# Optimization experiments

Hardware: AMD Instinct MI355X
Metric: run time of the kernel (lower is better)

The kernel has to match this reference:

```python
import jax, jax.numpy as jnp
import numpy as np

DIM = 96; NH = 3; WS = 7; SHIFT = 3; P = 5; H = 56; W = 56
HEAD = DIM // NH; SCALE = HEAD ** -0.5
NWH = H // WS; NWW = W // WS; NW = NWH * NWW
TP = P * NW                 # total prompts = 320
N = P + WS * WS             # tokens per window incl. prompts = 54
HIDDEN = int(DIM * 4.0)


def _rel_pos_index():
    coords = np.stack(np.meshgrid(np.arange(WS), np.arange(WS), indexing='ij'))
    cf = coords.reshape(2, -1)
    rel = (cf[:, :, None] - cf[:, None, :]).transpose(1, 2, 0).astype(np.int64)
    rel[..., 0] += WS - 1
    rel[..., 1] += WS - 1
    rel[..., 0] *= 2 * WS - 1
    return rel.sum(-1)  # (49, 49)


def _attn_mask():
    img = np.zeros((H, W))
    cnt = 0
    sl = (slice(0, -WS), slice(-WS, -SHIFT), slice(-SHIFT, None))
    for hs in sl:
        for wsl in sl:
            img[hs, wsl] = cnt
            cnt += 1
    mw = img.reshape(NWH, WS, NWW, WS).transpose(0, 2, 1, 3).reshape(NW, WS * WS)
    am = mw[:, None, :] - mw[:, :, None]
    am = np.where(am != 0, -100.0, 0.0).astype(np.float32)
    # zero-pad for prompt rows/cols, matching the torch code's cat of zeros
    return np.pad(am, ((0, 0), (P, 0), (P, 0)))  # (NW, N, N)


RPI = _rel_pos_index()
MASK = jnp.asarray(_attn_mask())


def _ln(x, g, b):
    m = x.mean(-1, keepdims=True)
    v = ((x - m) ** 2).mean(-1, keepdims=True)
    return (x - m) / jnp.sqrt(v + 1e-5) * g + b


def setup_inputs() -> dict:
    key = jax.random.key(0)
    ks = jax.random.split(key, 10)
    B = 64
    s = DIM ** -0.5
    return {
        'x': jax.random.normal(ks[0], (B, H * W + TP, DIM), jnp.float32),
        'norm1_g': jnp.ones((DIM,), jnp.float32),
        'norm1_b': jnp.zeros((DIM,), jnp.float32),
        'qkv_w': jax.random.normal(ks[1], (DIM, 3 * DIM), jnp.float32) * s,
        'qkv_b': jnp.zeros((3 * DIM,), jnp.float32),
        'rpb_table': jax.random.normal(ks[2], ((2 * WS - 1) ** 2, NH), jnp.float32) * 0.02,
        'proj_w': jax.random.normal(ks[3], (DIM, DIM), jnp.float32) * s,
        'proj_b': jnp.zeros((DIM,), jnp.float32),
        'norm2_g': jnp.ones((DIM,), jnp.float32),
        'norm2_b': jnp.zeros((DIM,), jnp.float32),
        'fc1_w': jax.random.normal(ks[4], (DIM, HIDDEN), jnp.float32) * s,
        'fc1_b': jnp.zeros((HIDDEN,), jnp.float32),
        'fc2_w': jax.random.normal(ks[5], (HIDDEN, DIM), jnp.float32) * (HIDDEN ** -0.5),
        'fc2_b': jnp.zeros((DIM,), jnp.float32),
    }


def _block(x, norm1_g, norm1_b, qkv_w, qkv_b, rpb_table, proj_w, proj_b,
           norm2_g, norm2_b, fc1_w, fc1_b, fc2_w, fc2_b):
    B = x.shape[0]
    shortcut = x
    xn = _ln(x, norm1_g, norm1_b)

    prompt = xn[:, :TP, :]                       # (B, NW*P, C)
    feat = xn[:, TP:, :].reshape(B, H, W, DIM)
    feat = jnp.roll(feat, (-SHIFT, -SHIFT), (1, 2))

    # window partition -> (B*NW, WS*WS, C)
    xw = feat.reshape(B, NWH, WS, NWW, WS, DIM).transpose(0, 1, 3, 2, 4, 5)
    xw = xw.reshape(B * NW, WS * WS, DIM)
    # prepend per-window prompts
    xw = jnp.concatenate([prompt.reshape(B * NW, P, DIM), xw], axis=1)  # (B*NW, N, C)

    # attention
    qkv = (xw @ qkv_w + qkv_b).reshape(B * NW, N, 3, NH, HEAD).transpose(2, 0, 3, 1, 4)
    q, k, v = qkv[0] * SCALE, qkv[1], qkv[2]     # (B*NW, NH, N, HEAD)
    attn = jnp.einsum('bhnd,bhmd->bhnm', q, k)

    bias = rpb_table[RPI.reshape(-1)].reshape(WS * WS, WS * WS, NH).transpose(2, 0, 1)
    bias = jnp.pad(bias, ((0, 0), (P, 0), (P, 0)))  # (NH, N, N)
    attn = attn + bias[None]

    attn = attn.reshape(B, NW, NH, N, N) + MASK[None, :, None]
    attn = jax.nn.softmax(attn.reshape(B * NW, NH, N, N), axis=-1)

    out = jnp.einsum('bhnm,bhmd->bhnd', attn, v).transpose(0, 2, 1, 3).reshape(B * NW, N, DIM)
    out = out @ proj_w + proj_b

    prompt_out = out[:, :P, :].reshape(B, TP, DIM)
    fo = out[:, P:, :].reshape(B, NWH, NWW, WS, WS, DIM).transpose(0, 1, 3, 2, 4, 5)
    fo = fo.reshape(B, H, W, DIM)
    fo = jnp.roll(fo, (SHIFT, SHIFT), (1, 2))

    y = jnp.concatenate([prompt_out, fo.reshape(B, H * W, DIM)], axis=1)
    y = shortcut + y

    h = _ln(y, norm2_g, norm2_b)
    h = jax.nn.gelu(h @ fc1_w + fc1_b, approximate=False)
    y = y + (h @ fc2_w + fc2_b)
    return y


def reference(x, norm1_g, norm1_b, qkv_w, qkv_b, rpb_table, proj_w, proj_b,
              norm2_g, norm2_b, fc1_w, fc1_b, fc2_w, fc2_b):
    return _block(x, norm1_g, norm1_b, qkv_w, qkv_b, rpb_table, proj_w, proj_b,
                  norm2_g, norm2_b, fc1_w, fc1_b, fc2_w, fc2_b)
```

## Files before the change

### kernel.cpp

```cpp
#include <hip/hip_runtime.h>
#include <cmath>

typedef __bf16 bf16x8 __attribute__((ext_vector_type(8)));
typedef float  f32x4  __attribute__((ext_vector_type(4)));

#define MFMA16(a,b,c) __builtin_amdgcn_mfma_f32_16x16x32_bf16((a),(b),(c),0,0,0)

#define SCALE_Q 0.17677669529663687f

#define KST 104
#define VP  68


__global__ __launch_bounds__(256) void prep(const float* __restrict__ qkv_w,
                                            const float* __restrict__ proj_w,
                                            const float* __restrict__ fc1_w,
                                            const float* __restrict__ fc2_w,
                                            const float* __restrict__ rpb,
                                            __bf16* __restrict__ ws,
                                            float* __restrict__ tbl)
{
    int i = blockIdx.x * 256 + threadIdx.x;
    {
        int j = i;
        if (j < 27648) {
            int c = j / 96, k = j % 96;
            float v = qkv_w[k * 288 + c];
            if (c < 96) v *= SCALE_Q;
            ws[j] = (__bf16)v;
        } else if ((j -= 27648) < 9216) {
            int c = j / 96, k = j % 96;
            ws[27648 + j] = (__bf16)proj_w[k * 96 + c];
        } else if ((j -= 9216) < 36864) {
            int c = j / 96, k = j % 96;
            ws[36864 + j] = (__bf16)fc1_w[k * 384 + c];
        } else if ((j -= 36864) < 36864) {
            int c = j / 384, k = j % 384;
            ws[73728 + j] = (__bf16)fc2_w[k * 96 + c];
        }
    }
    if (i < 49152) {
        int n = i & 63, m = (i >> 6) & 63, h = (i >> 12) % 3, cls = i / 12288;
        float v;
        if (m >= 54) {
            v = -1e30f;
        } else {
            v = 0.f;
            if (n >= 5 && n < 54 && m >= 5) {
                int an = n - 5, am = m - 5;
                int iy = an / 7, ix = an % 7, jy = am / 7, jx = am % 7;
                v = rpb[((iy - jy + 6) * 13 + (ix - jx + 6)) * 3 + h];
                int whp = cls >> 1, wwp = cls & 1;
                int idn = (whp ? (iy < 4 ? 1 : 2) : 0) * 3 + (wwp ? (ix < 4 ? 1 : 2) : 0);
                int idm = (whp ? (jy < 4 ? 1 : 2) : 0) * 3 + (wwp ? (jx < 4 ? 1 : 2) : 0);
                if (idn != idm) v -= 100.f;
            }
        }
        tbl[i] = v;
    }
}

__device__ __forceinline__ int src_index(int b, int w, int wh, int ww, int t)
{
    if (t < 5) return b * 3456 + w * 5 + t;
    int a = t - 5;
    int hi = wh * 7 + a / 7 + 3; if (hi >= 56) hi -= 56;
    int wi = ww * 7 + a % 7 + 3; if (wi >= 56) wi -= 56;
    return b * 3456 + 320 + hi * 56 + wi;
}

__global__ __launch_bounds__(256, 2) void block_fused(const float* __restrict__ x,
                                                  const float* __restrict__ n1g, const float* __restrict__ n1b,
                                                  const float* __restrict__ qkvb, const float* __restrict__ tbl,
                                                  const float* __restrict__ projb,
                                                  const float* __restrict__ n2g, const float* __restrict__ n2b,
                                                  const float* __restrict__ fc1b, const float* __restrict__ fc2b,
                                                  const __bf16* __restrict__ wqkvT, const __bf16* __restrict__ wprojT,
                                                  const __bf16* __restrict__ w1T, const __bf16* __restrict__ w2T,
                                                  float* __restrict__ out)
{
    __shared__ __align__(16) char smem[79360];

    const int tid  = threadIdx.x;
    const int lane = tid & 63;
    const int wv   = tid >> 6;
    const int l15  = lane & 15;
    const int quad = lane >> 4;

    const int g  = blockIdx.x;
    const int b  = g >> 5;
    const int wp = g & 31;

    const int trow = wv * 16 + l15;

    __bf16* kt[2];  __bf16* vTp[2];  __bf16* sw[2];  float* obf[2];
    int wI[2], whI[2], wwI[2], clsI[2], tsrc[2];
    #pragma unroll
    for (int wx = 0; wx < 2; wx++) {
        kt[wx]  = (__bf16*)(smem + wx * 13312);
        vTp[wx] = (__bf16*)(smem + 26624 + wx * 13056);
        sw[wx]  = (__bf16*)(smem + 52736 + (wv * 2 + wx) * 3328);
        obf[wx] = (float*)(smem + wx * 25600);
        int w = wp * 2 + wx;
        wI[wx] = w;  whI[wx] = w >> 3;  wwI[wx] = w & 7;
        clsI[wx] = ((whI[wx] == 7) ? 2 : 0) + ((wwI[wx] == 7) ? 1 : 0);
        tsrc[wx] = src_index(b, w, whI[wx], wwI[wx], trow < 54 ? trow : 53);
    }

    bf16x8 xnfr[2][3];
    {
        float xv[2][24];
        #pragma unroll
        for (int wx = 0; wx < 2; wx++) {
            if (trow < 54) {
                const float* xr = x + (size_t)tsrc[wx] * 96 + quad * 8;
                #pragma unroll
                for (int ks = 0; ks < 3; ks++) {
                    float4 a0 = *(const float4*)(xr + ks * 32);
                    float4 a1 = *(const float4*)(xr + ks * 32 + 4);
                    float* p = xv[wx] + ks * 8;
                    p[0]=a0.x; p[1]=a0.y; p[2]=a0.z; p[3]=a0.w;
                    p[4]=a1.x; p[5]=a1.y; p[6]=a1.z; p[7]=a1.w;
                }
            } else {
                #pragma unroll
                for (int j = 0; j < 24; j++) xv[wx][j] = 0.f;
            }
        }
        float s[2] = {0.f, 0.f}, sq[2] = {0.f, 0.f};
        #pragma unroll
        for (int wx = 0; wx < 2; wx++)
            #pragma unroll
            for (int j = 0; j < 24; j++) { s[wx] += xv[wx][j]; sq[wx] += xv[wx][j] * xv[wx][j]; }
        #pragma unroll
        for (int wx = 0; wx < 2; wx++) { s[wx] += __shfl_xor(s[wx], 16, 64); sq[wx] += __shfl_xor(sq[wx], 16, 64); }
        #pragma unroll
        for (int wx = 0; wx < 2; wx++) { s[wx] += __shfl_xor(s[wx], 32, 64); sq[wx] += __shfl_xor(sq[wx], 32, 64); }
        float mean[2], rstd[2];
        #pragma unroll
        for (int wx = 0; wx < 2; wx++) {
            mean[wx] = s[wx] * (1.f / 96.f);
            rstd[wx] = rsqrtf(sq[wx] * (1.f / 96.f) - mean[wx] * mean[wx] + 1e-5f);
        }
        float keep = (trow < 54) ? 1.f : 0.f;
        #pragma unroll
        for (int ks = 0; ks < 3; ks++) {
            const float* gp = n1g + ks * 32 + quad * 8;
            const float* bp = n1b + ks * 32 + quad * 8;
            float4 g0 = *(const float4*)(gp), g1 = *(const float4*)(gp + 4);
            float4 b0 = *(const float4*)(bp), b1 = *(const float4*)(bp + 4);
            float gg[8] = {g0.x,g0.y,g0.z,g0.w,g1.x,g1.y,g1.z,g1.w};
            float bb[8] = {b0.x,b0.y,b0.z,b0.w,b1.x,b1.y,b1.z,b1.w};
            #pragma unroll
            for (int wx = 0; wx < 2; wx++)
                #pragma unroll
                for (int j = 0; j < 8; j++)
                    xnfr[wx][ks][j] = (__bf16)(((xv[wx][ks*8+j] - mean[wx]) * rstd[wx] * gg[j] + bb[j]) * keep);
        }
    }

    #pragma unroll
    for (int nt = 0; nt < 6; nt++) {
        const __bf16* br = wqkvT + (size_t)(nt * 16 + l15) * 96 + quad * 8;
        bf16x8 bf0 = *(const bf16x8*)(br);
        bf16x8 bf1 = *(const bf16x8*)(br + 32);
        bf16x8 bf2 = *(const bf16x8*)(br + 64);
        int col = nt * 16 + l15;
        float bias = qkvb[col] * SCALE_Q;
        #pragma unroll
        for (int wx = 0; wx < 2; wx++) {
            f32x4 acc = {0.f, 0.f, 0.f, 0.f};
            acc = MFMA16(xnfr[wx][0], bf0, acc);
            acc = MFMA16(xnfr[wx][1], bf1, acc);
            acc = MFMA16(xnfr[wx][2], bf2, acc);
            #pragma unroll
            for (int r = 0; r < 4; r++)
                sw[wx][(quad * 4 + r) * KST + col] = (__bf16)(acc[r] + bias);
        }
    }
    bf16x8 aq[2][3];
    #pragma unroll
    for (int wx = 0; wx < 2; wx++)
        #pragma unroll
        for (int h = 0; h < 3; h++)
            aq[wx][h] = *(const bf16x8*)(sw[wx] + l15 * KST + h * 32 + quad * 8);
    #pragma unroll
    for (int nt = 6; nt < 18; nt++) {
        const __bf16* br = wqkvT + (size_t)(nt * 16 + l15) * 96 + quad * 8;
        bf16x8 bf0 = *(const bf16x8*)(br);
        bf16x8 bf1 = *(const bf16x8*)(br + 32);
        bf16x8 bf2 = *(const bf16x8*)(br + 64);
        int col = nt * 16 + l15;
        float bias = qkvb[col];
        #pragma unroll
        for (int wx = 0; wx < 2; wx++) {
            f32x4 acc = {0.f, 0.f, 0.f, 0.f};
            acc = MFMA16(xnfr[wx][0], bf0, acc);
            acc = MFMA16(xnfr[wx][1], bf1, acc);
            acc = MFMA16(xnfr[wx][2], bf2, acc);
            if (nt < 12) {
                int kc = col - 96;
                #pragma unroll
                for (int r = 0; r < 4; r++)
                    kt[wx][(wv * 16 + quad * 4 + r) * KST + kc] = (__bf16)(acc[r] + bias);
            } else {
                int vc = col - 192;
                #pragma unroll
                for (int r = 0; r < 4; r++)
                    vTp[wx][vc * VP + (wv * 16 + quad * 4 + r)] = (__bf16)(acc[r] + bias);
            }
        }
    }
    __syncthreads();

    f32x4 oacc[2][6];
    #pragma unroll
    for (int wx = 0; wx < 2; wx++)
        #pragma unroll
        for (int i = 0; i < 6; i++) oacc[wx][i] = (f32x4){0.f, 0.f, 0.f, 0.f};

    #pragma unroll
    for (int h = 0; h < 3; h++) {
        float schv[2][4][4];
        #pragma unroll
        for (int wx = 0; wx < 2; wx++) {
            const float* tbT = tbl + (size_t)(clsI[wx] * 3 + h) * 4096;
            #pragma unroll
            for (int nt = 0; nt < 4; nt++) {
                bf16x8 bk = *(const bf16x8*)(kt[wx] + (nt * 16 + l15) * KST + h * 32 + quad * 8);
                f32x4 c = {0.f, 0.f, 0.f, 0.f};
                c = MFMA16(aq[wx][h], bk, c);
                float4 tv = *(const float4*)(tbT + (l15 + 16 * nt) * 64 + wv * 16 + quad * 4);
                schv[wx][nt][0] = c[0] + tv.x;
                schv[wx][nt][1] = c[1] + tv.y;
                schv[wx][nt][2] = c[2] + tv.z;
                schv[wx][nt][3] = c[3] + tv.w;
            }
        }
        #pragma unroll
        for (int r = 0; r < 4; r++) {
            float mx[2], e0[2], e1[2], e2[2], e3[2], sum[2];
            #pragma unroll
            for (int wx = 0; wx < 2; wx++)
                mx[wx] = fmaxf(fmaxf(schv[wx][0][r], schv[wx][1][r]), fmaxf(schv[wx][2][r], schv[wx][3][r]));
            #pragma unroll
            for (int d = 1; d < 16; d <<= 1)
                #pragma unroll
                for (int wx = 0; wx < 2; wx++) mx[wx] = fmaxf(mx[wx], __shfl_xor(mx[wx], d, 16));
            #pragma unroll
            for (int wx = 0; wx < 2; wx++) {
                e0[wx] = __expf(schv[wx][0][r] - mx[wx]);
                e1[wx] = __expf(schv[wx][1][r] - mx[wx]);
                e2[wx] = __expf(schv[wx][2][r] - mx[wx]);
                e3[wx] = __expf(schv[wx][3][r] - mx[wx]);
                sum[wx] = e0[wx] + e1[wx] + e2[wx] + e3[wx];
            }
            #pragma unroll
            for (int d = 1; d < 16; d <<= 1)
                #pragma unroll
                for (int wx = 0; wx < 2; wx++) sum[wx] += __shfl_xor(sum[wx], d, 16);
            #pragma unroll
            for (int wx = 0; wx < 2; wx++) {
                float inv = 1.f / sum[wx];
                __bf16* prw = sw[wx] + (quad * 4 + r) * VP + l15;
                prw[0]  = (__bf16)(e0[wx] * inv);
                prw[16] = (__bf16)(e1[wx] * inv);
                prw[32] = (__bf16)(e2[wx] * inv);
                prw[48] = (__bf16)(e3[wx] * inv);
            }
        }
        bf16x8 pa0[2], pa1[2];
        #pragma unroll
        for (int wx = 0; wx < 2; wx++) {
            pa0[wx] = *(const bf16x8*)(sw[wx] + l15 * VP + quad * 8);
            pa1[wx] = *(const bf16x8*)(sw[wx] + l15 * VP + 32 + quad * 8);
        }
        #pragma unroll
        for (int wx = 0; wx < 2; wx++)
            #pragma unroll
            for (int dt = 0; dt < 2; dt++) {
                const __bf16* vr = vTp[wx] + (h * 32 + dt * 16 + l15) * VP + quad * 8;
                f32x4 acc = oacc[wx][h * 2 + dt];
                acc = MFMA16(pa0[wx], *(const bf16x8*)(vr), acc);
                acc = MFMA16(pa1[wx], *(const bf16x8*)(vr + 32), acc);
                oacc[wx][h * 2 + dt] = acc;
            }
    }

    #pragma unroll
    for (int wx = 0; wx < 2; wx++)
        #pragma unroll
        for (int i = 0; i < 6; i++) {
            int colb = i * 16 + l15;
            #pragma unroll
            for (int r = 0; r < 4; r++)
                sw[wx][(quad * 4 + r) * KST + colb] = (__bf16)oacc[wx][i][r];
        }
    bf16x8 ofr[2][3];
    #pragma unroll
    for (int wx = 0; wx < 2; wx++)
        #pragma unroll
        for (int ks = 0; ks < 3; ks++)
            ofr[wx][ks] = *(const bf16x8*)(sw[wx] + l15 * KST + ks * 32 + quad * 8);

    __syncthreads();

    #pragma unroll
    for (int nt = 0; nt < 6; nt++) {
        const __bf16* br = wprojT + (size_t)(nt * 16 + l15) * 96 + quad * 8;
        bf16x8 bf0 = *(const bf16x8*)(br);
        bf16x8 bf1 = *(const bf16x8*)(br + 32);
        bf16x8 bf2 = *(const bf16x8*)(br + 64);
        int col = nt * 16 + l15;
        float pb = projb[col];
        #pragma unroll
        for (int wx = 0; wx < 2; wx++) {
            f32x4 acc = {0.f, 0.f, 0.f, 0.f};
            acc = MFMA16(ofr[wx][0], bf0, acc);
            acc = MFMA16(ofr[wx][1], bf1, acc);
            acc = MFMA16(ofr[wx][2], bf2, acc);
            #pragma unroll
            for (int r = 0; r < 4; r++)
                obf[wx][(wv * 16 + quad * 4 + r) * 100 + col] = acc[r] + pb;
        }
    }

    float yv[2][24];
    float s2[2] = {0.f, 0.f}, sq2[2] = {0.f, 0.f};
    #pragma unroll
    for (int wx = 0; wx < 2; wx++) {
        const float* xr = x + (size_t)tsrc[wx] * 96 + quad * 8;
        #pragma unroll
        for (int ks = 0; ks < 3; ks++) {
            float4 xa = *(const float4*)(xr + ks * 32);
            float4 xb = *(const float4*)(xr + ks * 32 + 4);
            float* ap = obf[wx] + trow * 100 + ks * 32 + quad * 8;
            float* yp = yv[wx] + ks * 8;
            yp[0] = xa.x + ap[0]; yp[1] = xa.y + ap[1]; yp[2] = xa.z + ap[2]; yp[3] = xa.w + ap[3];
            yp[4] = xb.x + ap[4]; yp[5] = xb.y + ap[5]; yp[6] = xb.z + ap[6]; yp[7] = xb.w + ap[7];
            #pragma unroll
            for (int j = 0; j < 8; j++) { s2[wx] += yp[j]; sq2[wx] += yp[j] * yp[j]; }
            ap[0] = yp[0]; ap[1] = yp[1]; ap[2] = yp[2]; ap[3] = yp[3];
            ap[4] = yp[4]; ap[5] = yp[5]; ap[6] = yp[6]; ap[7] = yp[7];
        }
    }
    #pragma unroll
    for (int wx = 0; wx < 2; wx++) { s2[wx] += __shfl_xor(s2[wx], 16, 64); sq2[wx] += __shfl_xor(sq2[wx], 16, 64); }
    #pragma unroll
    for (int wx = 0; wx < 2; wx++) { s2[wx] += __shfl_xor(s2[wx], 32, 64); sq2[wx] += __shfl_xor(sq2[wx], 32, 64); }
    float mean2[2], rstd2[2];
    #pragma unroll
    for (int wx = 0; wx < 2; wx++) {
        mean2[wx] = s2[wx] * (1.f / 96.f);
        rstd2[wx] = rsqrtf(sq2[wx] * (1.f / 96.f) - mean2[wx] * mean2[wx] + 1e-5f);
    }

    bf16x8 afr[2][3];
    #pragma unroll
    for (int ks = 0; ks < 3; ks++) {
        float4 g0 = *(const float4*)(n2g + ks * 32 + quad * 8);
        float4 g1 = *(const float4*)(n2g + ks * 32 + quad * 8 + 4);
        float4 b0 = *(const float4*)(n2b + ks * 32 + quad * 8);
        float4 b1 = *(const float4*)(n2b + ks * 32 + quad * 8 + 4);
        float gg[8] = {g0.x,g0.y,g0.z,g0.w,g1.x,g1.y,g1.z,g1.w};
        float bb[8] = {b0.x,b0.y,b0.z,b0.w,b1.x,b1.y,b1.z,b1.w};
        #pragma unroll
        for (int wx = 0; wx < 2; wx++)
            #pragma unroll
            for (int j = 0; j < 8; j++)
                afr[wx][ks][j] = (__bf16)((yv[wx][ks*8+j] - mean2[wx]) * rstd2[wx] * gg[j] + bb[j]);
    }

    bf16x8 hfr[2][12];
    #pragma unroll
    for (int np = 0; np < 12; np++) {
        #pragma unroll
        for (int u = 0; u < 2; u++) {
            int ntx = np * 2 + u;
            const __bf16* br = w1T + (size_t)(ntx * 16 + l15) * 96 + quad * 8;
            bf16x8 bf0 = *(const bf16x8*)(br);
            bf16x8 bf1 = *(const bf16x8*)(br + 32);
            bf16x8 bf2 = *(const bf16x8*)(br + 64);
            float fb = fc1b[ntx * 16 + l15];
            #pragma unroll
            for (int wx = 0; wx < 2; wx++) {
                f32x4 acc = {0.f, 0.f, 0.f, 0.f};
                acc = MFMA16(afr[wx][0], bf0, acc);
                acc = MFMA16(afr[wx][1], bf1, acc);
                acc = MFMA16(afr[wx][2], bf2, acc);
                #pragma unroll
                for (int r = 0; r < 4; r++) {
                    float v  = acc[r] + fb;
                    float u2 = -1.5957691216057308f * v * (1.f + 0.044715f * v * v);
                    float t  = __expf(u2);
                    float ge = v * __builtin_amdgcn_rcpf(1.f + t);
                    sw[wx][(quad * 4 + r) * 40 + u * 16 + l15] = (__bf16)ge;
                }
            }
        }
        #pragma unroll
        for (int wx = 0; wx < 2; wx++)
            hfr[wx][np] = *(const bf16x8*)(sw[wx] + l15 * 40 + quad * 8);
    }

    #pragma unroll
    for (int nt = 0; nt < 6; nt++) {
        int col = nt * 16 + l15;
        const __bf16* br = w2T + (size_t)col * 384 + quad * 8;
        float fb = fc2b[col];
        f32x4 acc0 = {0.f, 0.f, 0.f, 0.f};
        f32x4 acc1 = {0.f, 0.f, 0.f, 0.f};
        #pragma unroll
        for (int ks = 0; ks < 12; ks++) {
            bf16x8 bb = *(const bf16x8*)(br + ks * 32);
            acc0 = MFMA16(hfr[0][ks], bb, acc0);
            acc1 = MFMA16(hfr[1][ks], bb, acc1);
        }
        #pragma unroll
        for (int r = 0; r < 4; r++) {
            obf[0][(wv * 16 + quad * 4 + r) * 100 + col] += acc0[r] + fb;
            obf[1][(wv * 16 + quad * 4 + r) * 100 + col] += acc1[r] + fb;
        }
    }

    #pragma unroll
    for (int wx = 0; wx < 2; wx++)
        #pragma unroll
        for (int it = 0; it < 6; it++) {
            int i = it * 64 + lane;
            int rr = i / 24, seg = i - rr * 24;
            int row = wv * 16 + rr;
            if (row < 54) {
                int src = src_index(b, wI[wx], whI[wx], wwI[wx], row);
                const float* sp = obf[wx] + row * 100 + seg * 4;
                float4 v = make_float4(sp[0], sp[1], sp[2], sp[3]);
                *(float4*)(out + (size_t)src * 96 + seg * 4) = v;
            }
        }
}

extern "C" void kernel_launch(void* const* d_in, const int* in_sizes, int n_in,
                              void* d_out, int out_size, void* d_ws, size_t ws_size,
                              hipStream_t stream)
{
    const float* x      = (const float*)d_in[0];
    const float* n1g    = (const float*)d_in[1];
    const float* n1b    = (const float*)d_in[2];
    const float* qkv_w  = (const float*)d_in[3];
    const float* qkv_b  = (const float*)d_in[4];
    const float* rpb    = (const float*)d_in[5];
    const float* proj_w = (const float*)d_in[6];
    const float* proj_b = (const float*)d_in[7];
    const float* n2g    = (const float*)d_in[8];
    const float* n2b    = (const float*)d_in[9];
    const float* fc1_w  = (const float*)d_in[10];
    const float* fc1_b  = (const float*)d_in[11];
    const float* fc2_w  = (const float*)d_in[12];
    const float* fc2_b  = (const float*)d_in[13];

    __bf16* ws     = (__bf16*)d_ws;
    __bf16* wqkvT  = ws;
    __bf16* wprojT = ws + 27648;
    __bf16* w1T    = ws + 36864;
    __bf16* w2T    = ws + 73728;
    float*  tbl    = (float*)((char*)d_ws + 221184);

    float* out = (float*)d_out;

    hipLaunchKernelGGL(prep, dim3(432), dim3(256), 0, stream,
                       qkv_w, proj_w, fc1_w, fc2_w, rpb, ws, tbl);
    hipLaunchKernelGGL(block_fused, dim3(2048), dim3(256), 0, stream,
                       x, n1g, n1b, qkv_b, tbl, proj_b, n2g, n2b, fc1_b, fc2_b,
                       wqkvT, wprojT, w1T, w2T, out);
}
```

Baseline: 357.4 us.

## Swap MFMA operand order to keep row-major token outputs in registers

Swaps the A/B operands of most MFMAs so each lane holds four consecutive output columns of one token row. This allows packed bf16x4 LDS stores, keeps the projection and residual outputs in registers instead of an fp32 LDS staging buffer, and writes the final output straight from registers. The softmax now reduces across lanes with two cross-quad shuffles instead of four 16-lane ones. fc1 and fc2 are interleaved so fc2 accumulates chunk by chunk without holding all hidden fragments, and one __syncthreads is dropped. The cost is higher register pressure from the acc2 and yv arrays, and the bias table is re-indexed to match the transposed score layout.

```diff
diff --git a/kernel.cpp b/kernel.cpp
--- a/kernel.cpp
+++ b/kernel.cpp
@@ -2,11 +2,13 @@
 #include <cmath>
 
 typedef __bf16 bf16x8 __attribute__((ext_vector_type(8)));
+typedef __bf16 bf16x4 __attribute__((ext_vector_type(4)));
 typedef float  f32x4  __attribute__((ext_vector_type(4)));
 
 #define MFMA16(a,b,c) __builtin_amdgcn_mfma_f32_16x16x32_bf16((a),(b),(c),0,0,0)
 
 #define SCALE_Q 0.17677669529663687f
+
 
 #define KST 104
 #define VP  68
@@ -40,14 +42,14 @@
         }
     }
     if (i < 49152) {
-        int n = i & 63, m = (i >> 6) & 63, h = (i >> 12) % 3, cls = i / 12288;
+        int k_ = i & 63, q_ = (i >> 6) & 63, h = (i >> 12) % 3, cls = i / 12288;
         float v;
-        if (m >= 54) {
+        if (k_ >= 54) {
             v = -1e30f;
         } else {
             v = 0.f;
-            if (n >= 5 && n < 54 && m >= 5) {
-                int an = n - 5, am = m - 5;
+            if (q_ >= 5 && q_ < 54 && k_ >= 5) {
+                int an = q_ - 5, am = k_ - 5;
                 int iy = an / 7, ix = an % 7, jy = am / 7, jx = am % 7;
                 v = rpb[((iy - jy + 6) * 13 + (ix - jx + 6)) * 3 + h];
                 int whp = cls >> 1, wwp = cls & 1;
@@ -93,14 +95,13 @@
 
     const int trow = wv * 16 + l15;
 
-    __bf16* kt[2];  __bf16* vTp[2];  __bf16* sw[2];  float* obf[2];
+    __bf16* kt[2];  __bf16* vTp[2];  __bf16* sw[2];
     int wI[2], whI[2], wwI[2], clsI[2], tsrc[2];
     #pragma unroll
     for (int wx = 0; wx < 2; wx++) {
         kt[wx]  = (__bf16*)(smem + wx * 13312);
         vTp[wx] = (__bf16*)(smem + 26624 + wx * 13056);
         sw[wx]  = (__bf16*)(smem + 52736 + (wv * 2 + wx) * 3328);
-        obf[wx] = (float*)(smem + wx * 25600);
         int w = wp * 2 + wx;
         wI[wx] = w;  whI[wx] = w >> 3;  wwI[wx] = w & 7;
         clsI[wx] = ((whI[wx] == 7) ? 2 : 0) + ((wwI[wx] == 7) ? 1 : 0);
@@ -136,46 +137,47 @@
         for (int wx = 0; wx < 2; wx++) { s[wx] += __shfl_xor(s[wx], 16, 64); sq[wx] += __shfl_xor(sq[wx], 16, 64); }
         #pragma unroll
         for (int wx = 0; wx < 2; wx++) { s[wx] += __shfl_xor(s[wx], 32, 64); sq[wx] += __shfl_xor(sq[wx], 32, 64); }
-        float mean[2], rstd[2];
-        #pragma unroll
-        for (int wx = 0; wx < 2; wx++) {
-            mean[wx] = s[wx] * (1.f / 96.f);
-            rstd[wx] = rsqrtf(sq[wx] * (1.f / 96.f) - mean[wx] * mean[wx] + 1e-5f);
-        }
         float keep = (trow < 54) ? 1.f : 0.f;
         #pragma unroll
-        for (int ks = 0; ks < 3; ks++) {
-            const float* gp = n1g + ks * 32 + quad * 8;
-            const float* bp = n1b + ks * 32 + quad * 8;
-            float4 g0 = *(const float4*)(gp), g1 = *(const float4*)(gp + 4);
-            float4 b0 = *(const float4*)(bp), b1 = *(const float4*)(bp + 4);
-            float gg[8] = {g0.x,g0.y,g0.z,g0.w,g1.x,g1.y,g1.z,g1.w};
-            float bb[8] = {b0.x,b0.y,b0.z,b0.w,b1.x,b1.y,b1.z,b1.w};
-            #pragma unroll
-            for (int wx = 0; wx < 2; wx++)
+        for (int wx = 0; wx < 2; wx++) {
+            float mean = s[wx] * (1.f / 96.f);
+            float rstd = rsqrtf(sq[wx] * (1.f / 96.f) - mean * mean + 1e-5f);
+            #pragma unroll
+            for (int ks = 0; ks < 3; ks++) {
+                const float* gp = n1g + ks * 32 + quad * 8;
+                const float* bp = n1b + ks * 32 + quad * 8;
+                float4 g0 = *(const float4*)(gp), g1 = *(const float4*)(gp + 4);
+                float4 b0 = *(const float4*)(bp), b1 = *(const float4*)(bp + 4);
+                float gg[8] = {g0.x,g0.y,g0.z,g0.w,g1.x,g1.y,g1.z,g1.w};
+                float bb[8] = {b0.x,b0.y,b0.z,b0.w,b1.x,b1.y,b1.z,b1.w};
                 #pragma unroll
                 for (int j = 0; j < 8; j++)
-                    xnfr[wx][ks][j] = (__bf16)(((xv[wx][ks*8+j] - mean[wx]) * rstd[wx] * gg[j] + bb[j]) * keep);
-        }
-    }
-
-    #pragma unroll
-    for (int nt = 0; nt < 6; nt++) {
+                    xnfr[wx][ks][j] = (__bf16)(((xv[wx][ks*8+j] - mean) * rstd * gg[j] + bb[j]) * keep);
+            }
+        }
+    }
+
+    #pragma unroll
+    for (int nt = 0; nt < 12; nt++) {
         const __bf16* br = wqkvT + (size_t)(nt * 16 + l15) * 96 + quad * 8;
-        bf16x8 bf0 = *(const bf16x8*)(br);
-        bf16x8 bf1 = *(const bf16x8*)(br + 32);
-        bf16x8 bf2 = *(const bf16x8*)(br + 64);
-        int col = nt * 16 + l15;
-        float bias = qkvb[col] * SCALE_Q;
+        bf16x8 b0 = *(const bf16x8*)(br);
+        bf16x8 b1 = *(const bf16x8*)(br + 32);
+        bf16x8 b2 = *(const bf16x8*)(br + 64);
+        float4 bias4 = *(const float4*)(qkvb + nt * 16 + quad * 4);
+        if (nt < 6) { bias4.x *= SCALE_Q; bias4.y *= SCALE_Q; bias4.z *= SCALE_Q; bias4.w *= SCALE_Q; }
         #pragma unroll
         for (int wx = 0; wx < 2; wx++) {
             f32x4 acc = {0.f, 0.f, 0.f, 0.f};
-            acc = MFMA16(xnfr[wx][0], bf0, acc);
-            acc = MFMA16(xnfr[wx][1], bf1, acc);
-            acc = MFMA16(xnfr[wx][2], bf2, acc);
-            #pragma unroll
-            for (int r = 0; r < 4; r++)
-                sw[wx][(quad * 4 + r) * KST + col] = (__bf16)(acc[r] + bias);
+            acc = MFMA16(b0, xnfr[wx][0], acc);
+            acc = MFMA16(b1, xnfr[wx][1], acc);
+            acc = MFMA16(b2, xnfr[wx][2], acc);
+            bf16x4 pk;
+            pk[0] = (__bf16)(acc[0] + bias4.x);
+            pk[1] = (__bf16)(acc[1] + bias4.y);
+            pk[2] = (__bf16)(acc[2] + bias4.z);
+            pk[3] = (__bf16)(acc[3] + bias4.w);
+            if (nt < 6) *(bf16x4*)(sw[wx] + l15 * KST + nt * 16 + quad * 4) = pk;
+            else        *(bf16x4*)(kt[wx] + (size_t)trow * KST + (nt - 6) * 16 + quad * 4) = pk;
         }
     }
     bf16x8 aq[2][3];
@@ -184,31 +186,27 @@
         #pragma unroll
         for (int h = 0; h < 3; h++)
             aq[wx][h] = *(const bf16x8*)(sw[wx] + l15 * KST + h * 32 + quad * 8);
-    #pragma unroll
-    for (int nt = 6; nt < 18; nt++) {
+
+    #pragma unroll
+    for (int nt = 12; nt < 18; nt++) {
         const __bf16* br = wqkvT + (size_t)(nt * 16 + l15) * 96 + quad * 8;
-        bf16x8 bf0 = *(const bf16x8*)(br);
-        bf16x8 bf1 = *(const bf16x8*)(br + 32);
-        bf16x8 bf2 = *(const bf16x8*)(br + 64);
-        int col = nt * 16 + l15;
-        float bias = qkvb[col];
+        bf16x8 b0 = *(const bf16x8*)(br);
+        bf16x8 b1 = *(const bf16x8*)(br + 32);
+        bf16x8 b2 = *(const bf16x8*)(br + 64);
+        float bias = qkvb[nt * 16 + l15];
+        int vc = nt * 16 + l15 - 192;
         #pragma unroll
         for (int wx = 0; wx < 2; wx++) {
             f32x4 acc = {0.f, 0.f, 0.f, 0.f};
-            acc = MFMA16(xnfr[wx][0], bf0, acc);
-            acc = MFMA16(xnfr[wx][1], bf1, acc);
-            acc = MFMA16(xnfr[wx][2], bf2, acc);
-            if (nt < 12) {
-                int kc = col - 96;
-                #pragma unroll
-                for (int r = 0; r < 4; r++)
-                    kt[wx][(wv * 16 + quad * 4 + r) * KST + kc] = (__bf16)(acc[r] + bias);
-            } else {
-                int vc = col - 192;
-                #pragma unroll
-                for (int r = 0; r < 4; r++)
-                    vTp[wx][vc * VP + (wv * 16 + quad * 4 + r)] = (__bf16)(acc[r] + bias);
-            }
+            acc = MFMA16(xnfr[wx][0], b0, acc);
+            acc = MFMA16(xnfr[wx][1], b1, acc);
+            acc = MFMA16(xnfr[wx][2], b2, acc);
+            bf16x4 pk;
+            pk[0] = (__bf16)(acc[0] + bias);
+            pk[1] = (__bf16)(acc[1] + bias);
+            pk[2] = (__bf16)(acc[2] + bias);
+            pk[3] = (__bf16)(acc[3] + bias);
+            *(bf16x4*)(vTp[wx] + (size_t)vc * VP + wv * 16 + quad * 4) = pk;
         }
     }
     __syncthreads();
@@ -221,107 +219,99 @@
 
     #pragma unroll
     for (int h = 0; h < 3; h++) {
-        float schv[2][4][4];
-        #pragma unroll
-        for (int wx = 0; wx < 2; wx++) {
-            const float* tbT = tbl + (size_t)(clsI[wx] * 3 + h) * 4096;
+        float sv[2][4][4];
+        #pragma unroll
+        for (int wx = 0; wx < 2; wx++) {
+            const float* tbh = tbl + (size_t)(clsI[wx] * 3 + h) * 4096 + trow * 64 + quad * 4;
             #pragma unroll
             for (int nt = 0; nt < 4; nt++) {
-                bf16x8 bk = *(const bf16x8*)(kt[wx] + (nt * 16 + l15) * KST + h * 32 + quad * 8);
+                bf16x8 ak = *(const bf16x8*)(kt[wx] + (nt * 16 + l15) * KST + h * 32 + quad * 8);
                 f32x4 c = {0.f, 0.f, 0.f, 0.f};
-                c = MFMA16(aq[wx][h], bk, c);
-                float4 tv = *(const float4*)(tbT + (l15 + 16 * nt) * 64 + wv * 16 + quad * 4);
-                schv[wx][nt][0] = c[0] + tv.x;
-                schv[wx][nt][1] = c[1] + tv.y;
-                schv[wx][nt][2] = c[2] + tv.z;
-                schv[wx][nt][3] = c[3] + tv.w;
-            }
-        }
-        #pragma unroll
-        for (int r = 0; r < 4; r++) {
-            float mx[2], e0[2], e1[2], e2[2], e3[2], sum[2];
-            #pragma unroll
-            for (int wx = 0; wx < 2; wx++)
-                mx[wx] = fmaxf(fmaxf(schv[wx][0][r], schv[wx][1][r]), fmaxf(schv[wx][2][r], schv[wx][3][r]));
-            #pragma unroll
-            for (int d = 1; d < 16; d <<= 1)
-                #pragma unroll
-                for (int wx = 0; wx < 2; wx++) mx[wx] = fmaxf(mx[wx], __shfl_xor(mx[wx], d, 16));
-            #pragma unroll
-            for (int wx = 0; wx < 2; wx++) {
-                e0[wx] = __expf(schv[wx][0][r] - mx[wx]);
-                e1[wx] = __expf(schv[wx][1][r] - mx[wx]);
-                e2[wx] = __expf(schv[wx][2][r] - mx[wx]);
-                e3[wx] = __expf(schv[wx][3][r] - mx[wx]);
-                sum[wx] = e0[wx] + e1[wx] + e2[wx] + e3[wx];
-            }
-            #pragma unroll
-            for (int d = 1; d < 16; d <<= 1)
-                #pragma unroll
-                for (int wx = 0; wx < 2; wx++) sum[wx] += __shfl_xor(sum[wx], d, 16);
-            #pragma unroll
-            for (int wx = 0; wx < 2; wx++) {
-                float inv = 1.f / sum[wx];
-                __bf16* prw = sw[wx] + (quad * 4 + r) * VP + l15;
-                prw[0]  = (__bf16)(e0[wx] * inv);
-                prw[16] = (__bf16)(e1[wx] * inv);
-                prw[32] = (__bf16)(e2[wx] * inv);
-                prw[48] = (__bf16)(e3[wx] * inv);
-            }
-        }
-        bf16x8 pa0[2], pa1[2];
-        #pragma unroll
-        for (int wx = 0; wx < 2; wx++) {
-            pa0[wx] = *(const bf16x8*)(sw[wx] + l15 * VP + quad * 8);
-            pa1[wx] = *(const bf16x8*)(sw[wx] + l15 * VP + 32 + quad * 8);
-        }
-        #pragma unroll
-        for (int wx = 0; wx < 2; wx++)
+                c = MFMA16(ak, aq[wx][h], c);
+                float4 tv = *(const float4*)(tbh + nt * 16);
+                sv[wx][nt][0] = c[0] + tv.x;
+                sv[wx][nt][1] = c[1] + tv.y;
+                sv[wx][nt][2] = c[2] + tv.z;
+                sv[wx][nt][3] = c[3] + tv.w;
+            }
+        }
+        #pragma unroll
+        for (int wx = 0; wx < 2; wx++) {
+            float mx = sv[wx][0][0];
+            #pragma unroll
+            for (int nt = 0; nt < 4; nt++)
+                #pragma unroll
+                for (int r = 0; r < 4; r++) mx = fmaxf(mx, sv[wx][nt][r]);
+            mx = fmaxf(mx, __shfl_xor(mx, 16, 64));
+            mx = fmaxf(mx, __shfl_xor(mx, 32, 64));
+            float ps[4][4]; float sum = 0.f;
+            #pragma unroll
+            for (int nt = 0; nt < 4; nt++)
+                #pragma unroll
+                for (int r = 0; r < 4; r++) { ps[nt][r] = __expf(sv[wx][nt][r] - mx); sum += ps[nt][r]; }
+            sum += __shfl_xor(sum, 16, 64);
+            sum += __shfl_xor(sum, 32, 64);
+            float inv = 1.f / sum;
+            #pragma unroll
+            for (int nt = 0; nt < 4; nt++) {
+                bf16x4 pk;
+                pk[0] = (__bf16)(ps[nt][0] * inv);
+                pk[1] = (__bf16)(ps[nt][1] * inv);
+                pk[2] = (__bf16)(ps[nt][2] * inv);
+                pk[3] = (__bf16)(ps[nt][3] * inv);
+                *(bf16x4*)(sw[wx] + l15 * KST + nt * 16 + quad * 4) = pk;
+            }
+        }
+        #pragma unroll
+        for (int wx = 0; wx < 2; wx++) {
+            bf16x8 pa0 = *(const bf16x8*)(sw[wx] + l15 * KST + quad * 8);
+            bf16x8 pa1 = *(const bf16x8*)(sw[wx] + l15 * KST + 32 + quad * 8);
             #pragma unroll
             for (int dt = 0; dt < 2; dt++) {
-                const __bf16* vr = vTp[wx] + (h * 32 + dt * 16 + l15) * VP + quad * 8;
+                const __bf16* vr = vTp[wx] + (h * 32 + dt * 16 + l15) * VP;
                 f32x4 acc = oacc[wx][h * 2 + dt];
-                acc = MFMA16(pa0[wx], *(const bf16x8*)(vr), acc);
-                acc = MFMA16(pa1[wx], *(const bf16x8*)(vr + 32), acc);
+                acc = MFMA16(*(const bf16x8*)(vr + quad * 8), pa0, acc);
+                acc = MFMA16(*(const bf16x8*)(vr + 32 + quad * 8), pa1, acc);
                 oacc[wx][h * 2 + dt] = acc;
             }
-    }
-
-    #pragma unroll
-    for (int wx = 0; wx < 2; wx++)
+        }
+    }
+
+    bf16x8 ofr[2][3];
+    #pragma unroll
+    for (int wx = 0; wx < 2; wx++) {
         #pragma unroll
         for (int i = 0; i < 6; i++) {
-            int colb = i * 16 + l15;
-            #pragma unroll
-            for (int r = 0; r < 4; r++)
-                sw[wx][(quad * 4 + r) * KST + colb] = (__bf16)oacc[wx][i][r];
-        }
-    bf16x8 ofr[2][3];
-    #pragma unroll
-    for (int wx = 0; wx < 2; wx++)
+            bf16x4 pk;
+            pk[0] = (__bf16)oacc[wx][i][0];
+            pk[1] = (__bf16)oacc[wx][i][1];
+            pk[2] = (__bf16)oacc[wx][i][2];
+            pk[3] = (__bf16)oacc[wx][i][3];
+            *(bf16x4*)(sw[wx] + l15 * KST + i * 16 + quad * 4) = pk;
+        }
         #pragma unroll
         for (int ks = 0; ks < 3; ks++)
             ofr[wx][ks] = *(const bf16x8*)(sw[wx] + l15 * KST + ks * 32 + quad * 8);
-
-    __syncthreads();
-
+    }
+
+    float av[2][24];
     #pragma unroll
     for (int nt = 0; nt < 6; nt++) {
         const __bf16* br = wprojT + (size_t)(nt * 16 + l15) * 96 + quad * 8;
-        bf16x8 bf0 = *(const bf16x8*)(br);
-        bf16x8 bf1 = *(const bf16x8*)(br + 32);
-        bf16x8 bf2 = *(const bf16x8*)(br + 64);
-        int col = nt * 16 + l15;
-        float pb = projb[col];
+        bf16x8 b0 = *(const bf16x8*)(br);
+        bf16x8 b1 = *(const bf16x8*)(br + 32);
+        bf16x8 b2 = *(const bf16x8*)(br + 64);
+        float4 pb = *(const float4*)(projb + nt * 16 + quad * 4);
         #pragma unroll
         for (int wx = 0; wx < 2; wx++) {
             f32x4 acc = {0.f, 0.f, 0.f, 0.f};
-            acc = MFMA16(ofr[wx][0], bf0, acc);
-            acc = MFMA16(ofr[wx][1], bf1, acc);
-            acc = MFMA16(ofr[wx][2], bf2, acc);
-            #pragma unroll
-            for (int r = 0; r < 4; r++)
-                obf[wx][(wv * 16 + quad * 4 + r) * 100 + col] = acc[r] + pb;
+            acc = MFMA16(b0, ofr[wx][0], acc);
+            acc = MFMA16(b1, ofr[wx][1], acc);
+            acc = MFMA16(b2, ofr[wx][2], acc);
+            av[wx][nt*4+0] = acc[0] + pb.x;
+            av[wx][nt*4+1] = acc[1] + pb.y;
+            av[wx][nt*4+2] = acc[2] + pb.z;
+            av[wx][nt*4+3] = acc[3] + pb.w;
         }
     }
 
@@ -329,114 +319,105 @@
     float s2[2] = {0.f, 0.f}, sq2[2] = {0.f, 0.f};
     #pragma unroll
     for (int wx = 0; wx < 2; wx++) {
-        const float* xr = x + (size_t)tsrc[wx] * 96 + quad * 8;
-        #pragma unroll
-        for (int ks = 0; ks < 3; ks++) {
-            float4 xa = *(const float4*)(xr + ks * 32);
-            float4 xb = *(const float4*)(xr + ks * 32 + 4);
-            float* ap = obf[wx] + trow * 100 + ks * 32 + quad * 8;
-            float* yp = yv[wx] + ks * 8;
-            yp[0] = xa.x + ap[0]; yp[1] = xa.y + ap[1]; yp[2] = xa.z + ap[2]; yp[3] = xa.w + ap[3];
-            yp[4] = xb.x + ap[4]; yp[5] = xb.y + ap[5]; yp[6] = xb.z + ap[6]; yp[7] = xb.w + ap[7];
-            #pragma unroll
-            for (int j = 0; j < 8; j++) { s2[wx] += yp[j]; sq2[wx] += yp[j] * yp[j]; }
-            ap[0] = yp[0]; ap[1] = yp[1]; ap[2] = yp[2]; ap[3] = yp[3];
-            ap[4] = yp[4]; ap[5] = yp[5]; ap[6] = yp[6]; ap[7] = yp[7];
+        const float* xr = x + (size_t)tsrc[wx] * 96 + quad * 4;
+        #pragma unroll
+        for (int nt = 0; nt < 6; nt++) {
+            float4 xa = *(const float4*)(xr + nt * 16);
+            float* yp = yv[wx] + nt * 4;
+            yp[0] = xa.x + av[wx][nt*4+0];
+            yp[1] = xa.y + av[wx][nt*4+1];
+            yp[2] = xa.z + av[wx][nt*4+2];
+            yp[3] = xa.w + av[wx][nt*4+3];
+            #pragma unroll
+            for (int j = 0; j < 4; j++) { s2[wx] += yp[j]; sq2[wx] += yp[j] * yp[j]; }
         }
     }
     #pragma unroll
     for (int wx = 0; wx < 2; wx++) { s2[wx] += __shfl_xor(s2[wx], 16, 64); sq2[wx] += __shfl_xor(sq2[wx], 16, 64); }
     #pragma unroll
     for (int wx = 0; wx < 2; wx++) { s2[wx] += __shfl_xor(s2[wx], 32, 64); sq2[wx] += __shfl_xor(sq2[wx], 32, 64); }
-    float mean2[2], rstd2[2];
+
+    bf16x8 afr[2][3];
     #pragma unroll
     for (int wx = 0; wx < 2; wx++) {
-        mean2[wx] = s2[wx] * (1.f / 96.f);
-        rstd2[wx] = rsqrtf(sq2[wx] * (1.f / 96.f) - mean2[wx] * mean2[wx] + 1e-5f);
-    }
-
-    bf16x8 afr[2][3];
-    #pragma unroll
-    for (int ks = 0; ks < 3; ks++) {
-        float4 g0 = *(const float4*)(n2g + ks * 32 + quad * 8);
-        float4 g1 = *(const float4*)(n2g + ks * 32 + quad * 8 + 4);
-        float4 b0 = *(const float4*)(n2b + ks * 32 + quad * 8);
-        float4 b1 = *(const float4*)(n2b + ks * 32 + quad * 8 + 4);
-        float gg[8] = {g0.x,g0.y,g0.z,g0.w,g1.x,g1.y,g1.z,g1.w};
-        float bb[8] = {b0.x,b0.y,b0.z,b0.w,b1.x,b1.y,b1.z,b1.w};
-        #pragma unroll
-        for (int wx = 0; wx < 2; wx++)
-            #pragma unroll
-            for (int j = 0; j < 8; j++)
-                afr[wx][ks][j] = (__bf16)((yv[wx][ks*8+j] - mean2[wx]) * rstd2[wx] * gg[j] + bb[j]);
-    }
-
-    bf16x8 hfr[2][12];
+        float mean = s2[wx] * (1.f / 96.f);
+        float rstd = rsqrtf(sq2[wx] * (1.f / 96.f) - mean * mean + 1e-5f);
+        #pragma unroll
+        for (int nt = 0; nt < 6; nt++) {
+            float4 gg = *(const float4*)(n2g + nt * 16 + quad * 4);
+            float4 bb = *(const float4*)(n2b + nt * 16 + quad * 4);
+            bf16x4 pk;
+            pk[0] = (__bf16)((yv[wx][nt*4+0] - mean) * rstd * gg.x + bb.x);
+            pk[1] = (__bf16)((yv[wx][nt*4+1] - mean) * rstd * gg.y + bb.y);
+            pk[2] = (__bf16)((yv[wx][nt*4+2] - mean) * rstd * gg.z + bb.z);
+            pk[3] = (__bf16)((yv[wx][nt*4+3] - mean) * rstd * gg.w + bb.w);
+            *(bf16x4*)(sw[wx] + l15 * KST + nt * 16 + quad * 4) = pk;
+        }
+        #pragma unroll
+        for (int ks = 0; ks < 3; ks++)
+            afr[wx][ks] = *(const bf16x8*)(sw[wx] + l15 * KST + ks * 32 + quad * 8);
+    }
+
+    f32x4 acc2[2][6];
+    #pragma unroll
+    for (int wx = 0; wx < 2; wx++)
+        #pragma unroll
+        for (int nt = 0; nt < 6; nt++) acc2[wx][nt] = (f32x4){0.f, 0.f, 0.f, 0.f};
+
     #pragma unroll
     for (int np = 0; np < 12; np++) {
+        int reg = (np % 3) * 32;
         #pragma unroll
         for (int u = 0; u < 2; u++) {
             int ntx = np * 2 + u;
             const __bf16* br = w1T + (size_t)(ntx * 16 + l15) * 96 + quad * 8;
-            bf16x8 bf0 = *(const bf16x8*)(br);
-            bf16x8 bf1 = *(const bf16x8*)(br + 32);
-            bf16x8 bf2 = *(const bf16x8*)(br + 64);
-            float fb = fc1b[ntx * 16 + l15];
+            bf16x8 b0 = *(const bf16x8*)(br);
+            bf16x8 b1 = *(const bf16x8*)(br + 32);
+            bf16x8 b2 = *(const bf16x8*)(br + 64);
+            float4 fb = *(const float4*)(fc1b + ntx * 16 + quad * 4);
+            float fbv[4] = {fb.x, fb.y, fb.z, fb.w};
             #pragma unroll
             for (int wx = 0; wx < 2; wx++) {
                 f32x4 acc = {0.f, 0.f, 0.f, 0.f};
-                acc = MFMA16(afr[wx][0], bf0, acc);
-                acc = MFMA16(afr[wx][1], bf1, acc);
-                acc = MFMA16(afr[wx][2], bf2, acc);
+                acc = MFMA16(b0, afr[wx][0], acc);
+                acc = MFMA16(b1, afr[wx][1], acc);
+                acc = MFMA16(b2, afr[wx][2], acc);
+                bf16x4 pk;
                 #pragma unroll
                 for (int r = 0; r < 4; r++) {
-                    float v  = acc[r] + fb;
+                    float v  = acc[r] + fbv[r];
                     float u2 = -1.5957691216057308f * v * (1.f + 0.044715f * v * v);
                     float t  = __expf(u2);
-                    float ge = v * __builtin_amdgcn_rcpf(1.f + t);
-                    sw[wx][(quad * 4 + r) * 40 + u * 16 + l15] = (__bf16)ge;
+                    pk[r] = (__bf16)(v * __builtin_amdgcn_rcpf(1.f + t));
                 }
-            }
-        }
-        #pragma unroll
-        for (int wx = 0; wx < 2; wx++)
-            hfr[wx][np] = *(const bf16x8*)(sw[wx] + l15 * 40 + quad * 8);
+                *(bf16x4*)(sw[wx] + l15 * KST + reg + u * 16 + quad * 4) = pk;
+            }
+        }
+        bf16x8 hc0 = *(const bf16x8*)(sw[0] + l15 * KST + reg + quad * 8);
+        bf16x8 hc1 = *(const bf16x8*)(sw[1] + l15 * KST + reg + quad * 8);
+        #pragma unroll
+        for (int nt = 0; nt < 6; nt++) {
+            bf16x8 wb = *(const bf16x8*)(w2T + (size_t)(nt * 16 + l15) * 384 + np * 32 + quad * 8);
+            acc2[0][nt] = MFMA16(wb, hc0, acc2[0][nt]);
+            acc2[1][nt] = MFMA16(wb, hc1, acc2[1][nt]);
+        }
     }
 
     #pragma unroll
     for (int nt = 0; nt < 6; nt++) {
-        int col = nt * 16 + l15;
-        const __bf16* br = w2T + (size_t)col * 384 + quad * 8;
-        float fb = fc2b[col];
-        f32x4 acc0 = {0.f, 0.f, 0.f, 0.f};
-        f32x4 acc1 = {0.f, 0.f, 0.f, 0.f};
-        #pragma unroll
-        for (int ks = 0; ks < 12; ks++) {
-            bf16x8 bb = *(const bf16x8*)(br + ks * 32);
-            acc0 = MFMA16(hfr[0][ks], bb, acc0);
-            acc1 = MFMA16(hfr[1][ks], bb, acc1);
-        }
-        #pragma unroll
-        for (int r = 0; r < 4; r++) {
-            obf[0][(wv * 16 + quad * 4 + r) * 100 + col] += acc0[r] + fb;
-            obf[1][(wv * 16 + quad * 4 + r) * 100 + col] += acc1[r] + fb;
-        }
-    }
-
-    #pragma unroll
-    for (int wx = 0; wx < 2; wx++)
-        #pragma unroll
-        for (int it = 0; it < 6; it++) {
-            int i = it * 64 + lane;
-            int rr = i / 24, seg = i - rr * 24;
-            int row = wv * 16 + rr;
-            if (row < 54) {
-                int src = src_index(b, wI[wx], whI[wx], wwI[wx], row);
-                const float* sp = obf[wx] + row * 100 + seg * 4;
-                float4 v = make_float4(sp[0], sp[1], sp[2], sp[3]);
-                *(float4*)(out + (size_t)src * 96 + seg * 4) = v;
-            }
-        }
+        float4 fb = *(const float4*)(fc2b + nt * 16 + quad * 4);
+        #pragma unroll
+        for (int wx = 0; wx < 2; wx++) {
+            if (trow < 54) {
+                float4 o;
+                o.x = yv[wx][nt*4+0] + acc2[wx][nt][0] + fb.x;
+                o.y = yv[wx][nt*4+1] + acc2[wx][nt][1] + fb.y;
+                o.z = yv[wx][nt*4+2] + acc2[wx][nt][2] + fb.z;
+                o.w = yv[wx][nt*4+3] + acc2[wx][nt][3] + fb.w;
+                *(float4*)(out + (size_t)tsrc[wx] * 96 + nt * 16 + quad * 4) = o;
+            }
+        }
+    }
 }
 
 extern "C" void kernel_launch(void* const* d_in, const int* in_sizes, int n_in,
```

Result: no change. 358.5 us (+0.3%).
